# Optimization experiments

Hardware: AMD Instinct MI355X
Metric: run time of the kernel (lower is better)

The kernel has to match this reference:

```python
import jax, jax.numpy as jnp
import numpy as np


def _sobel_filters():
    # 3D Sobel kernels for x, y, z directions, shape (3, 1, 3, 3, 3) in OIDHW.
    x = np.array([[[-1, 0, 1], [-2, 0, 2], [-1, 0, 1]],
                  [[-2, 0, 2], [-4, 0, 4], [-2, 0, 2]],
                  [[-1, 0, 1], [-2, 0, 2], [-1, 0, 1]]], dtype=np.float32)
    y = np.array([[[1, 2, 1], [0, 0, 0], [-1, -2, -1]],
                  [[2, 4, 2], [0, 0, 0], [-2, -4, -2]],
                  [[1, 2, 1], [0, 0, 0], [-1, -2, -1]]], dtype=np.float32)
    z = np.array([[[1, 2, 1], [2, 4, 2], [1, 2, 1]],
                  [[0, 0, 0], [0, 0, 0], [0, 0, 0]],
                  [[-1, -2, -1], [-2, -4, -2], [-1, -2, -1]]], dtype=np.float32)
    return jnp.asarray(np.stack([x, y, z])[:, None])  # (3,1,3,3,3)


_FILTERS = _sobel_filters()
_EPS = 1e-10


def gradient3d(x):
    # x: [B,1,D,H,W] -> gradient magnitude [B,1,D,H,W].
    # Single conv with 3 output channels == three separate torch conv3d + concat.
    g = jax.lax.conv_general_dilated(
        x, _FILTERS, window_strides=(1, 1, 1),
        padding=[(1, 1), (1, 1), (1, 1)],
        dimension_numbers=('NCDHW', 'OIDHW', 'NCDHW'))  # [B,3,D,H,W]
    return jnp.sqrt(jnp.sum(g * g, axis=1, keepdims=True) + _EPS)


def setup_inputs() -> dict:
    key = jax.random.key(0)
    k1, k2, k3 = jax.random.split(key, 3)
    shape = (2, 1, 192, 192, 192)
    pred = jax.random.normal(k1, shape, dtype=jnp.float32)
    gt_dose = jax.random.normal(k2, shape, dtype=jnp.float32)
    body_mask = (jax.random.uniform(k3, shape) > 0.3).astype(jnp.float32)
    return {"pred": pred, "gt_dose": gt_dose, "body_mask": body_mask}


def reference(pred, gt_dose, body_mask):
    mse = jnp.square(pred - gt_dose) * body_mask
    mge = jnp.square(gradient3d(gt_dose) - gradient3d(pred)) * body_mask
    return jnp.mean(mse + jnp.tanh(mge) * mse)
```

## Files before the change

kernel.cpp:

```cpp
#include <hip/hip_runtime.h>
#include <math.h>

#define W 192
#define H 192
#define DEPTH 192
#define BATCH 2
#define TW 64
#define TH 8
#define DC 12
#define HW (H * W)
#define VOL ((size_t)DEPTH * HW)
#define LROW 72
#define LPLANE (LROW * 10)
#define NPAIR ((DC + 2) / 2)
#define NITEM 720
#define NBUF 3
#define BUFFLOATS 3072

__device__ __align__(16) float g_zero16[16] = {0.f};

__global__ __launch_bounds__(256) void sobel_loss_part(
    const float* __restrict__ pred, const float* __restrict__ gt,
    const float* __restrict__ mask, float* __restrict__ partials)
{
    __shared__ __align__(16) float lds[NBUF * BUFFLOATS];
    __shared__ float red[4];

    const int tid = threadIdx.x;
    const int tx = blockIdx.x % 3;
    const int ty = blockIdx.x / 3;
    const int w0 = tx * TW, h0 = ty * TH;
    const int d0 = blockIdx.y * DC;
    const size_t base = (size_t)blockIdx.z * VOL;

    const int wv  = tid >> 6;
    const int col = tid & 63;
    const size_t moff = base + (size_t)(h0 + 2 * wv) * W + (w0 + col);

    int it_ok[3], it_q[3];
    size_t it_goff[3];
    const float* it_src[3];
    #pragma unroll
    for (int k = 0; k < 3; ++k) {
        int j = tid + 256 * k;
        int jj = (j < NITEM) ? j : 0;
        int a = jj / 360; int pj = jj - a * 360;
        int q = pj / 180; int e = pj - q * 180;
        int r = e / 18;   int c = e - r * 18;
        int y  = h0 - 1 + r;
        int xf = w0 - 4 + 4 * c;
        it_ok[k]  = (j < NITEM) && ((unsigned)y < (unsigned)H) && ((unsigned)xf < (unsigned)W);
        it_goff[k] = it_ok[k] ? ((size_t)y * W + xf) : 0;
        it_q[k]    = q;
        it_src[k]  = a ? gt : pred;
    }

    typedef const __attribute__((address_space(1))) void GV;
    typedef __attribute__((address_space(3))) void LV;

    auto dma_pair = [&](int s) {
        float* bufp = lds + (s % NBUF) * BUFFLOATS;
        const int p0 = d0 - 1 + 2 * s;
        #pragma unroll
        for (int k = 0; k < 3; ++k) {
            const int p = p0 + it_q[k];
            const bool v = it_ok[k] && (p >= 0) && (p < DEPTH);
            const float* ga = v ? (it_src[k] + base + (size_t)p * HW + it_goff[k])
                               : g_zero16;
            __builtin_amdgcn_global_load_lds((GV*)ga,
                (LV*)(bufp + (((wv << 6) + (k << 8)) << 2)), 16, 0, 0);
        }
    };

    float2 Mn = make_float2(0.f, 0.f), Mn1 = make_float2(0.f, 0.f);
    float2 Mc, Mc1;
    auto load_mask = [&](int s) {
        const size_t p0 = moff + (size_t)(d0 + 2 * s - 2) * HW;
        Mn  = make_float2(mask[p0], mask[p0 + W]);
        Mn1 = make_float2(mask[p0 + HW], mask[p0 + HW + W]);
    };

    float dx[2][2][3], dy[2][2][3], sm[2][2][3], ct[2][2][2];
    #pragma unroll
    for (int a = 0; a < 2; ++a)
        #pragma unroll
        for (int o = 0; o < 2; ++o) {
            dx[a][o][0]=dx[a][o][1]=dx[a][o][2]=0.f;
            dy[a][o][0]=dy[a][o][1]=dy[a][o][2]=0.f;
            sm[a][o][0]=sm[a][o][1]=sm[a][o][2]=0.f;
            ct[a][o][0]=ct[a][o][1]=0.f;
        }
    float acc = 0.f;

    dma_pair(0);
    dma_pair(1);

    for (int s = 0; s < NPAIR; ++s) {
        if (s < NPAIR - 1) {
            asm volatile("s_waitcnt vmcnt(3)" ::: "memory");
        } else {
            asm volatile("s_waitcnt vmcnt(0)" ::: "memory");
        }
        __builtin_amdgcn_sched_barrier(0);
        __builtin_amdgcn_s_barrier();
        __builtin_amdgcn_sched_barrier(0);

        if (s + 2 < NPAIR) dma_pair(s + 2);

        Mc = Mn; Mc1 = Mn1;
        if (s + 1 < NPAIR) load_mask(s + 1);

        const float* buf = lds + (s % NBUF) * BUFFLOATS;

        #pragma unroll
        for (int q = 0; q < 2; ++q) {
            const int p = d0 - 1 + 2 * s + q;

            #pragma unroll
            for (int a = 0; a < 2; ++a) {
                const int ab = (a * 2 + q) * LPLANE + (2 * wv) * LROW + col + 3;
                float e[4][3];
                #pragma unroll
                for (int rr = 0; rr < 4; ++rr)
                    #pragma unroll
                    for (int d = 0; d < 3; ++d)
                        e[rr][d] = buf[ab + rr * LROW + d];

                float rs[4], rd[4];
                #pragma unroll
                for (int rr = 0; rr < 4; ++rr) {
                    rs[rr] = e[rr][0] + 2.f * e[rr][1] + e[rr][2];
                    rd[rr] = e[rr][2] - e[rr][0];
                }
                #pragma unroll
                for (int o = 0; o < 2; ++o) {
                    dx[a][o][0] = dx[a][o][1]; dx[a][o][1] = dx[a][o][2];
                    dx[a][o][2] = rd[o] + 2.f * rd[o+1] + rd[o+2];
                    sm[a][o][0] = sm[a][o][1]; sm[a][o][1] = sm[a][o][2];
                    sm[a][o][2] = rs[o] + 2.f * rs[o+1] + rs[o+2];
                    dy[a][o][0] = dy[a][o][1]; dy[a][o][1] = dy[a][o][2];
                    dy[a][o][2] = rs[o] - rs[o+2];
                    ct[a][o][0] = ct[a][o][1]; ct[a][o][1] = e[o+1][1];
                }
            }

            if (p >= d0 + 1) {
                const float2 M = q ? Mc1 : Mc;
                #pragma unroll
                for (int o = 0; o < 2; ++o) {
                    float gxa = dx[0][o][0] + 2.f * dx[0][o][1] + dx[0][o][2];
                    float gya = dy[0][o][0] + 2.f * dy[0][o][1] + dy[0][o][2];
                    float gza = sm[0][o][0] - sm[0][o][2];
                    float gxb = dx[1][o][0] + 2.f * dx[1][o][1] + dx[1][o][2];
                    float gyb = dy[1][o][0] + 2.f * dy[1][o][1] + dy[1][o][2];
                    float gzb = sm[1][o][0] - sm[1][o][2];
                    float ga = __builtin_amdgcn_sqrtf(gxa * gxa + gya * gya + gza * gza + 1e-10f);
                    float gb = __builtin_amdgcn_sqrtf(gxb * gxb + gyb * gyb + gzb * gzb + 1e-10f);
                    float m  = o ? M.y : M.x;
                    float dm = ct[0][o][0] - ct[1][o][0];
                    float mse = dm * dm * m;
                    float dg  = gb - ga;
                    float mge = dg * dg * m;
                    float ex = __expf(2.f * mge);
                    float t  = 1.f - 2.f * __builtin_amdgcn_rcpf(ex + 1.f);
                    acc += mse * (1.f + t);
                }
            }
        }
    }

    float v = acc;
    #pragma unroll
    for (int o = 32; o > 0; o >>= 1) v += __shfl_down(v, o, 64);
    if ((tid & 63) == 0) red[tid >> 6] = v;
    __syncthreads();
    if (tid == 0) {
        partials[(size_t)blockIdx.z * (gridDim.x * gridDim.y)
                 + (size_t)blockIdx.y * gridDim.x + blockIdx.x]
            = red[0] + red[1] + red[2] + red[3];
    }
}

__global__ __launch_bounds__(256) void reduce_final(
    const float* __restrict__ partials, int n, float* __restrict__ out)
{
    int tid = threadIdx.x;
    double s = 0.0;
    for (int i = tid; i < n; i += 256) s += (double)partials[i];
    #pragma unroll
    for (int o = 32; o > 0; o >>= 1) s += __shfl_down(s, o, 64);
    __shared__ double red[4];
    if ((tid & 63) == 0) red[tid >> 6] = s;
    __syncthreads();
    if (tid == 0) {
        double t = red[0] + red[1] + red[2] + red[3];
        const double ntot = (double)BATCH * (double)DEPTH * (double)H * (double)W;
        out[0] = (float)(t / ntot);
    }
}

extern "C" void kernel_launch(void* const* d_in, const int* in_sizes, int n_in,
                              void* d_out, int out_size, void* d_ws, size_t ws_size,
                              hipStream_t stream) {
    const float* pred = (const float*)d_in[0];
    const float* gt   = (const float*)d_in[1];
    const float* mask = (const float*)d_in[2];
    float* partials = (float*)d_ws;

    dim3 grid((W / TW) * (H / TH), DEPTH / DC, BATCH);
    sobel_loss_part<<<grid, 256, 0, stream>>>(pred, gt, mask, partials);

    int nparts = grid.x * grid.y * grid.z;
    reduce_final<<<1, 256, 0, stream>>>(partials, nparts, (float*)d_out);
}
```

Before: 186.8 us.

## Double tile height to 16 rows with 512 threads and two-stage LDS pipeline

Each block now covers a 64x16 tile using 512 threads, so the one-row halo above and below is a smaller share of the rows loaded and redundant global reads drop. The LDS ring goes from three buffers to two, and the prefetch depth falls from two pairs ahead to one, waiting on vmcnt(0) every step. The larger tile means fewer blocks and more LDS per block. The shallower prefetch may expose more memory latency.

```diff
diff --git a/kernel.cpp b/kernel.cpp
--- a/kernel.cpp
+++ b/kernel.cpp
@@ -6,25 +6,30 @@
 #define DEPTH 192
 #define BATCH 2
 #define TW 64
-#define TH 8
+#define TH 16
 #define DC 12
+#define NT 512
 #define HW (H * W)
 #define VOL ((size_t)DEPTH * HW)
 #define LROW 72
-#define LPLANE (LROW * 10)
+#define LROWS 18
+#define LPLANE (LROW * LROWS)
 #define NPAIR ((DC + 2) / 2)
-#define NITEM 720
-#define NBUF 3
-#define BUFFLOATS 3072
+#define NITEM 1296
+#define NBUF 2
+#define BUFFLOATS 6144
+#define GX ((W / TW) * (H / TH))
+#define GY (DEPTH / DC)
+#define NBLK (GX * GY * BATCH)
 
 __device__ __align__(16) float g_zero16[16] = {0.f};
 
-__global__ __launch_bounds__(256) void sobel_loss_part(
+__global__ __launch_bounds__(NT) void sobel_loss_part(
     const float* __restrict__ pred, const float* __restrict__ gt,
     const float* __restrict__ mask, float* __restrict__ partials)
 {
     __shared__ __align__(16) float lds[NBUF * BUFFLOATS];
-    __shared__ float red[4];
+    __shared__ float red[8];
 
     const int tid = threadIdx.x;
     const int tx = blockIdx.x % 3;
@@ -42,10 +47,10 @@
     const float* it_src[3];
     #pragma unroll
     for (int k = 0; k < 3; ++k) {
-        int j = tid + 256 * k;
+        int j = tid + NT * k;
         int jj = (j < NITEM) ? j : 0;
-        int a = jj / 360; int pj = jj - a * 360;
-        int q = pj / 180; int e = pj - q * 180;
+        int a = jj / 648; int pj = jj - a * 648;
+        int q = pj / 324; int e = pj - q * 324;
         int r = e / 18;   int c = e - r * 18;
         int y  = h0 - 1 + r;
         int xf = w0 - 4 + 4 * c;
@@ -59,7 +64,7 @@
     typedef __attribute__((address_space(3))) void LV;
 
     auto dma_pair = [&](int s) {
-        float* bufp = lds + (s % NBUF) * BUFFLOATS;
+        float* bufp = lds + (s & 1) * BUFFLOATS;
         const int p0 = d0 - 1 + 2 * s;
         #pragma unroll
         for (int k = 0; k < 3; ++k) {
@@ -68,7 +73,7 @@
             const float* ga = v ? (it_src[k] + base + (size_t)p * HW + it_goff[k])
                                : g_zero16;
             __builtin_amdgcn_global_load_lds((GV*)ga,
-                (LV*)(bufp + (((wv << 6) + (k << 8)) << 2)), 16, 0, 0);
+                (LV*)(bufp + (((wv << 6) + (k << 9)) << 2)), 16, 0, 0);
         }
     };
 
@@ -93,24 +98,20 @@
     float acc = 0.f;
 
     dma_pair(0);
-    dma_pair(1);
 
     for (int s = 0; s < NPAIR; ++s) {
-        if (s < NPAIR - 1) {
-            asm volatile("s_waitcnt vmcnt(3)" ::: "memory");
-        } else {
-            asm volatile("s_waitcnt vmcnt(0)" ::: "memory");
-        }
+        asm volatile("s_waitcnt vmcnt(0)" ::: "memory");
         __builtin_amdgcn_sched_barrier(0);
         __builtin_amdgcn_s_barrier();
         __builtin_amdgcn_sched_barrier(0);
 
-        if (s + 2 < NPAIR) dma_pair(s + 2);
-
         Mc = Mn; Mc1 = Mn1;
-        if (s + 1 < NPAIR) load_mask(s + 1);
-
-        const float* buf = lds + (s % NBUF) * BUFFLOATS;
+        if (s + 1 < NPAIR) {
+            load_mask(s + 1);
+            dma_pair(s + 1);
+        }
+
+        const float* buf = lds + (s & 1) * BUFFLOATS;
 
         #pragma unroll
         for (int q = 0; q < 2; ++q) {
@@ -175,9 +176,11 @@
     if ((tid & 63) == 0) red[tid >> 6] = v;
     __syncthreads();
     if (tid == 0) {
-        partials[(size_t)blockIdx.z * (gridDim.x * gridDim.y)
-                 + (size_t)blockIdx.y * gridDim.x + blockIdx.x]
-            = red[0] + red[1] + red[2] + red[3];
+        float bs = 0.f;
+        #pragma unroll
+        for (int i = 0; i < 8; ++i) bs += red[i];
+        partials[(size_t)blockIdx.z * (GX * GY)
+                 + (size_t)blockIdx.y * GX + blockIdx.x] = bs;
     }
 }
 
@@ -207,9 +210,8 @@
     const float* mask = (const float*)d_in[2];
     float* partials = (float*)d_ws;
 
-    dim3 grid((W / TW) * (H / TH), DEPTH / DC, BATCH);
-    sobel_loss_part<<<grid, 256, 0, stream>>>(pred, gt, mask, partials);
-
-    int nparts = grid.x * grid.y * grid.z;
-    reduce_final<<<1, 256, 0, stream>>>(partials, nparts, (float*)d_out);
+    dim3 grid(GX, GY, BATCH);
+    sobel_loss_part<<<grid, NT, 0, stream>>>(pred, gt, mask, partials);
+
+    reduce_final<<<1, 256, 0, stream>>>(partials, NBLK, (float*)d_out);
 }
```

After: 193.5 us. +3.6%, slower.
